# Optimization experiments

Hardware: AMD Instinct MI355X
Metric: run time of the kernel (lower is better)

## Reference

```python
import jax, jax.numpy as jnp
import numpy as np
import math

N_HEADS = 12


def setup_inputs() -> dict:
    key = jax.random.key(0)
    ks = jax.random.split(key, 6)
    B, S, DIM = 4, 2048, 768
    h = jax.random.normal(ks[0], (B, S, DIM), dtype=jnp.float32)
    attn_mask = jnp.ones((B, 1, 1, S), dtype=jnp.int32)
    scale = 1.0 / math.sqrt(DIM)
    wq = jax.random.normal(ks[1], (DIM, DIM), dtype=jnp.float32) * scale
    wk = jax.random.normal(ks[2], (DIM, DIM), dtype=jnp.float32) * scale
    wv = jax.random.normal(ks[3], (DIM, DIM), dtype=jnp.float32) * scale
    wo = jax.random.normal(ks[4], (DIM, DIM), dtype=jnp.float32) * scale
    return {"h": h, "attn_mask": attn_mask, "wq": wq, "wk": wk, "wv": wv, "wo": wo}


def reference(h, attn_mask, wq, wk, wv, wo):
    B, S, dim = h.shape
    H = N_HEADS
    D = dim // H
    qk_scale = 1.0 / math.sqrt(D)
    # NOTE: original uses .view(B, H, S, D) on the [B, S, H*D] projection —
    # a raw reshape, NOT the usual (B,S,H,D)->(B,H,S,D) transpose. Reproduce exactly.
    hq = (h @ wq.T).reshape(B, H, S, D)
    hk = (h @ wk.T).reshape(B, H, S, D)
    hv = (h @ wv.T).reshape(B, H, S, D)
    scores = jnp.einsum("bhqd,bhkd->bhqk", hq, hk) * qk_scale  # [B,H,S,S]
    scores = jnp.where(attn_mask == 0, -jnp.inf, scores)
    attn = jax.nn.softmax(scores.astype(jnp.float32), axis=-1)
    ctx = jnp.einsum("bhqk,bhkd->bhqd", attn, hv)  # [B,H,S,D]
    # dropout is identity in eval mode
    ctx = ctx.reshape(B, S, H * D)
    return ctx @ wo.T
```

## Files before the change

### kernel.cpp

```cpp
#include <hip/hip_runtime.h>
#include <math.h>

typedef __bf16 bf16x8 __attribute__((ext_vector_type(8)));
typedef float  f32x4  __attribute__((ext_vector_type(4)));
typedef float  f32x16 __attribute__((ext_vector_type(16)));

#define MFMA16(a, b, c) __builtin_amdgcn_mfma_f32_16x16x32_bf16((a), (b), (c), 0, 0, 0)
#define MFMA32(a, b, c) __builtin_amdgcn_mfma_f32_32x32x16_bf16((a), (b), (c), 0, 0, 0)

__device__ __forceinline__ unsigned short f2bf(float f) {
    unsigned int u = __float_as_uint(f);
    u += 0x7fffu + ((u >> 16) & 1u);
    return (unsigned short)(u >> 16);
}

__device__ __forceinline__ void gll16(const unsigned short* g, unsigned short* l) {
    __builtin_amdgcn_global_load_lds(
        (const __attribute__((address_space(1))) unsigned int*)g,
        (__attribute__((address_space(3))) unsigned int*)l, 16, 0, 0);
}

__global__ __launch_bounds__(256) void convert_kernel(
    const float* __restrict__ h, const float* __restrict__ wq,
    const float* __restrict__ wk, const float* __restrict__ wv,
    const float* __restrict__ wo,
    unsigned short* __restrict__ hb, unsigned short* __restrict__ wb)
{
    const int NH4 = 1572864;
    const int NW4 = 147456;
    int i4 = blockIdx.x * 256 + threadIdx.x;
    const float4* src;
    unsigned short* dst;
    int off;
    float sc = 1.0f;
    if (i4 < NH4) {
        src = (const float4*)h; dst = hb; off = i4;
    } else {
        int j = i4 - NH4;
        int w = j / NW4;
        off = j - w * NW4;
        const float* s = (w == 0) ? wq : (w == 1) ? wk : (w == 2) ? wv : wo;
        if (w == 0) sc = 0.18033688011112042f;
        src = (const float4*)s;
        dst = wb + w * 589824;
    }
    float4 v = src[off];
    ushort4 o;
    o.x = f2bf(v.x * sc); o.y = f2bf(v.y * sc);
    o.z = f2bf(v.z * sc); o.w = f2bf(v.w * sc);
    ((ushort4*)dst)[off] = o;
}

template <typename OutT>
__global__ __launch_bounds__(256) void gemm_bt(
    const unsigned short* __restrict__ A,
    const unsigned short* __restrict__ Bm,
    OutT* __restrict__ C)
{
    constexpr int K = 768, N = 768;
    __shared__ unsigned short As[2][128 * 32];
    __shared__ unsigned short Bs[2][128 * 32];
    const unsigned short* Bz = Bm + (size_t)blockIdx.z * N * K;
    OutT* Cz = C + (size_t)blockIdx.z * 8192 * N;

    const int tid  = threadIdx.x;
    const int bm   = blockIdx.x * 128, bn = blockIdx.y * 128;
    const int wave = tid >> 6, lane = tid & 63;
    const int wm   = (wave & 1) * 64, wn = (wave >> 1) * 64;
    const int l16  = lane & 15, quad = lane >> 4;

    const int sr  = tid >> 2;
    const int sp8 = ((tid & 3) ^ (sr & 3)) * 8;
    const int slot8 = (quad ^ (l16 & 3)) * 8;

    auto stage = [&](int k0, int bi) {
        gll16(A  + (size_t)(bm + sr) * K      + k0 + sp8, As[bi] + tid * 8);
        gll16(A  + (size_t)(bm + 64 + sr) * K + k0 + sp8, As[bi] + 2048 + tid * 8);
        gll16(Bz + (size_t)(bn + sr) * K      + k0 + sp8, Bs[bi] + tid * 8);
        gll16(Bz + (size_t)(bn + 64 + sr) * K + k0 + sp8, Bs[bi] + 2048 + tid * 8);
    };

    f32x4 acc[4][4] = {};

    stage(0, 0);
    __syncthreads();

    for (int i = 0; i < 24; i++) {
        const int cur = i & 1;
        if (i < 23) stage((i + 1) * 32, cur ^ 1);

        bf16x8 af[4], bfv[4];
        #pragma unroll
        for (int ii = 0; ii < 4; ii++)
            af[ii] = *(const bf16x8*)(As[cur] + (wm + ii * 16 + l16) * 32 + slot8);
        #pragma unroll
        for (int jj = 0; jj < 4; jj++)
            bfv[jj] = *(const bf16x8*)(Bs[cur] + (wn + jj * 16 + l16) * 32 + slot8);
        #pragma unroll
        for (int ii = 0; ii < 4; ii++)
            #pragma unroll
            for (int jj = 0; jj < 4; jj++)
                acc[ii][jj] = MFMA16(af[ii], bfv[jj], acc[ii][jj]);

        __syncthreads();
    }

    #pragma unroll
    for (int ii = 0; ii < 4; ii++) {
        #pragma unroll
        for (int jj = 0; jj < 4; jj++) {
            int row0 = bm + wm + ii * 16 + quad * 4;
            int col  = bn + wn + jj * 16 + l16;
            #pragma unroll
            for (int r = 0; r < 4; r++) {
                float v = acc[ii][jj][r];
                size_t idx = (size_t)(row0 + r) * N + col;
                if constexpr (sizeof(OutT) == 2) Cz[idx] = f2bf(v);
                else                             Cz[idx] = v;
            }
        }
    }
}

__global__ __launch_bounds__(256) void vtrans_kernel(
    const unsigned short* __restrict__ Vg,
    unsigned short* __restrict__ vt)
{
    constexpr int LDT = 72;
    __shared__ unsigned short Ts[64 * LDT];
    const int b = blockIdx.z, hh = blockIdx.y, kp0 = blockIdx.x * 64;
    const int tid = threadIdx.x;
    const size_t boff = (size_t)b * (24576 * 64);
    const int rowV0 = hh * 2048 + kp0;

    #pragma unroll
    for (int rep = 0; rep < 2; rep++) {
        int idx = rep * 256 + tid;
        int r = idx >> 3, dp = (idx & 7) * 8;
        uint4 v = *(const uint4*)(Vg + boff + (size_t)(rowV0 + r) * 64 + dp);
        unsigned short tmp[8];
        *(uint4*)tmp = v;
        #pragma unroll
        for (int i = 0; i < 8; i++) Ts[(dp + i) * LDT + r] = tmp[i];
    }
    __syncthreads();
    unsigned short* vtb = vt + ((size_t)(b * 12 + hh)) * 64 * 2048;
    #pragma unroll
    for (int rep = 0; rep < 2; rep++) {
        int idx = rep * 256 + tid;
        int d = idx >> 3, kp = (idx & 7) * 8;
        uint4 v = *(const uint4*)(Ts + d * LDT + kp);
        *(uint4*)(vtb + (size_t)d * 2048 + kp0 + kp) = v;
    }
}

__global__ __launch_bounds__(256) void attn_kernel(
    const unsigned short* __restrict__ Qg,
    const unsigned short* __restrict__ Kg,
    const unsigned short* __restrict__ vt,
    const int* __restrict__ mask,
    unsigned short* __restrict__ Og)
{
    __shared__ unsigned short Qs[128 * 64];
    __shared__ unsigned short Ks[2][64 * 64];
    __shared__ unsigned short Vs[2][64 * 64];
    __shared__ unsigned long long msh[32];

    const int b = blockIdx.z, hh = blockIdx.y, qt = blockIdx.x;
    const int tid  = threadIdx.x;
    const int wave = tid >> 6, lane = tid & 63;
    const int c31  = lane & 31, h = lane >> 5;
    const size_t boff = (size_t)b * (24576 * 64);
    const int rowQ0 = hh * 2048 + qt * 128;
    const int rowK0 = hh * 2048;
    const unsigned short* vtg = vt + ((size_t)(b * 12 + hh)) * 64 * 2048;
    const int sw = c31 & 7;

    const int srow = tid >> 3;
    const int sch8 = ((tid & 7) ^ (srow & 7)) * 8;

    auto stageKV = [&](int kt, int bi) {
        #pragma unroll
        for (int i = 0; i < 2; i++) {
            int row = i * 32 + srow;
            gll16(Kg  + boff + (size_t)(rowK0 + kt * 64 + row) * 64 + sch8,
                  Ks[bi] + i * 2048 + tid * 8);
            gll16(vtg + (size_t)row * 2048 + kt * 64 + sch8,
                  Vs[bi] + i * 2048 + tid * 8);
        }
    };

    #pragma unroll
    for (int i = 0; i < 4; i++) {
        int row = i * 32 + srow;
        gll16(Qg + boff + (size_t)(rowQ0 + row) * 64 + sch8, Qs + i * 2048 + tid * 8);
    }
    stageKV(0, 0);

    {
        const int4 a = *(const int4*)(mask + b * 2048 + tid * 8);
        const int4 c = *(const int4*)(mask + b * 2048 + tid * 8 + 4);
        unsigned char byte =
            (a.x != 0 ? 1u : 0u)       | (a.y != 0 ? 2u : 0u) |
            (a.z != 0 ? 4u : 0u)       | (a.w != 0 ? 8u : 0u) |
            (c.x != 0 ? 16u : 0u)      | (c.y != 0 ? 32u : 0u) |
            (c.z != 0 ? 64u : 0u)      | (c.w != 0 ? 128u : 0u);
        ((unsigned char*)msh)[tid] = byte;
    }
    __syncthreads();

    bf16x8 qf[4];
    #pragma unroll
    for (int c = 0; c < 4; c++) {
        int ch = (2 * c + h) ^ sw;
        qf[c] = *(const bf16x8*)(Qs + (wave * 32 + c31) * 64 + ch * 8);
    }

    f32x16 acc[2] = {};
    float l_run = 0.f;

    for (int kt = 0; kt < 32; kt++) {
        const int cur = kt & 1;
        if (kt < 31) stageKV(kt + 1, cur ^ 1);

        const unsigned long long am = msh[kt];

        f32x16 sT[2];
        #pragma unroll
        for (int t2 = 0; t2 < 2; t2++) {
            f32x16 z = {};
            #pragma unroll
            for (int c = 0; c < 4; c++) {
                int ch = (2 * c + h) ^ sw;
                bf16x8 kf = *(const bf16x8*)(Ks[cur] + (t2 * 32 + c31) * 64 + ch * 8);
                z = MFMA32(kf, qf[c], z);
            }
            sT[t2] = z;
        }

        unsigned int p01[2][4], p23[2][4];
        if (am == ~0ull) {
            #pragma unroll
            for (int t2 = 0; t2 < 2; t2++) {
                #pragma unroll
                for (int s = 0; s < 4; s++) {
                    float e0 = __builtin_amdgcn_exp2f(sT[t2][4*s+0]);
                    float e1 = __builtin_amdgcn_exp2f(sT[t2][4*s+1]);
                    float e2 = __builtin_amdgcn_exp2f(sT[t2][4*s+2]);
                    float e3 = __builtin_amdgcn_exp2f(sT[t2][4*s+3]);
                    unsigned int u0 = __float_as_uint(e0) & 0xffff0000u;
                    unsigned int u1 = __float_as_uint(e1) & 0xffff0000u;
                    unsigned int u2 = __float_as_uint(e2) & 0xffff0000u;
                    unsigned int u3 = __float_as_uint(e3) & 0xffff0000u;
                    l_run += __uint_as_float(u0) + __uint_as_float(u1)
                           + __uint_as_float(u2) + __uint_as_float(u3);
                    p01[t2][s] = __builtin_amdgcn_perm(u1, u0, 0x07060302u);
                    p23[t2][s] = __builtin_amdgcn_perm(u3, u2, 0x07060302u);
                }
            }
        } else {
            #pragma unroll
            for (int t2 = 0; t2 < 2; t2++) {
                #pragma unroll
                for (int s = 0; s < 4; s++) {
                    unsigned int nib = (unsigned int)(am >> (t2 * 32 + 8 * s + 4 * h)) & 0xFu;
                    float e0 = __builtin_amdgcn_exp2f(sT[t2][4*s+0]);
                    float e1 = __builtin_amdgcn_exp2f(sT[t2][4*s+1]);
                    float e2 = __builtin_amdgcn_exp2f(sT[t2][4*s+2]);
                    float e3 = __builtin_amdgcn_exp2f(sT[t2][4*s+3]);
                    e0 = (nib & 1u) ? e0 : 0.f;
                    e1 = (nib & 2u) ? e1 : 0.f;
                    e2 = (nib & 4u) ? e2 : 0.f;
                    e3 = (nib & 8u) ? e3 : 0.f;
                    unsigned int u0 = __float_as_uint(e0) & 0xffff0000u;
                    unsigned int u1 = __float_as_uint(e1) & 0xffff0000u;
                    unsigned int u2 = __float_as_uint(e2) & 0xffff0000u;
                    unsigned int u3 = __float_as_uint(e3) & 0xffff0000u;
                    l_run += __uint_as_float(u0) + __uint_as_float(u1)
                           + __uint_as_float(u2) + __uint_as_float(u3);
                    p01[t2][s] = __builtin_amdgcn_perm(u1, u0, 0x07060302u);
                    p23[t2][s] = __builtin_amdgcn_perm(u3, u2, 0x07060302u);
                }
            }
        }

        #pragma unroll
        for (int q = 0; q < 4; q++) {
            int t = q >> 1, p = q & 1;
            unsigned int L01 = h ? p01[t][2*p+1] : p01[t][2*p];
            unsigned int L23 = h ? p23[t][2*p+1] : p23[t][2*p];
            unsigned int pre01 = h ? p01[t][2*p] : p01[t][2*p+1];
            unsigned int pre23 = h ? p23[t][2*p] : p23[t][2*p+1];
            unsigned int P01 = (unsigned int)__shfl((int)pre01, lane ^ 32, 64);
            unsigned int P23 = (unsigned int)__shfl((int)pre23, lane ^ 32, 64);
            uint4 pfu;
            pfu.x = h ? P01 : L01;
            pfu.y = h ? P23 : L23;
            pfu.z = h ? L01 : P01;
            pfu.w = h ? L23 : P23;
            bf16x8 pf;
            __builtin_memcpy(&pf, &pfu, 16);
            #pragma unroll
            for (int nt = 0; nt < 2; nt++) {
                int ch = (2 * q + h) ^ sw;
                bf16x8 vf = *(const bf16x8*)(Vs[cur] + (nt * 32 + c31) * 64 + ch * 8);
                acc[nt] = MFMA32(pf, vf, acc[nt]);
            }
        }

        __syncthreads();
    }

    float lt = l_run + __shfl_xor(l_run, 32, 64);
    float linv = 1.0f / lt;
    #pragma unroll
    for (int reg = 0; reg < 16; reg++) {
        int rowfn = (reg & 3) + 8 * (reg >> 2) + 4 * h;
        float li = __shfl(linv, rowfn, 64);
        int row = rowQ0 + wave * 32 + rowfn;
        #pragma unroll
        for (int nt = 0; nt < 2; nt++)
            Og[boff + (size_t)row * 64 + nt * 32 + c31] = f2bf(acc[nt][reg] * li);
    }
}

extern "C" void kernel_launch(void* const* d_in, const int* in_sizes, int n_in,
                              void* d_out, int out_size, void* d_ws, size_t ws_size,
                              hipStream_t stream)
{
    const float* h    = (const float*)d_in[0];
    const int*   mask = (const int*)d_in[1];
    const float* wq   = (const float*)d_in[2];
    const float* wk   = (const float*)d_in[3];
    const float* wv   = (const float*)d_in[4];
    const float* wo   = (const float*)d_in[5];

    unsigned short* hb  = (unsigned short*)d_ws;
    unsigned short* wb  = hb + 6291456;
    unsigned short* qkv = wb + 4 * 589824;
    unsigned short* ctx = qkv + (size_t)3 * 6291456;

    convert_kernel<<<8448, 256, 0, stream>>>(h, wq, wk, wv, wo, hb, wb);
    gemm_bt<unsigned short><<<dim3(64, 6, 3), 256, 0, stream>>>(hb, wb, qkv);
    vtrans_kernel<<<dim3(32, 12, 4), 256, 0, stream>>>(qkv + (size_t)2 * 6291456, hb);
    attn_kernel<<<dim3(16, 12, 4), 256, 0, stream>>>(
        qkv, qkv + 6291456, hb, mask, ctx);
    gemm_bt<float><<<dim3(64, 6, 1), 256, 0, stream>>>(
        ctx, wb + (size_t)3 * 589824, (float*)d_out);
}
```

Measured before the change: 257.1 us.

## Use packed bf16 convert, permlane32 swap, and MFMA row-sum for softmax denominator

Replaces the manual truncate-and-perm bf16 packing of exponentials with v_cvt_pk_bf16_f32, which also switches rounding from truncation to round-to-nearest. Replaces the cross-half __shfl exchange with v_permlane32_swap_b32. Computes the softmax denominator by running an extra MFMA of P against a ones vector instead of scalar per-lane accumulation and shuffles. This removes VALU adds, bpermute traffic and the final shuffle, at the cost of one extra MFMA per step and a 16-register accumulator.

```diff
diff --git a/kernel.cpp b/kernel.cpp
--- a/kernel.cpp
+++ b/kernel.cpp
@@ -217,7 +217,10 @@
     }
 
     f32x16 acc[2] = {};
-    float l_run = 0.f;
+    f32x16 acc_l  = {};
+    bf16x8 onesf;
+    #pragma unroll
+    for (int i = 0; i < 8; i++) onesf[i] = (__bf16)1.0f;
 
     for (int kt = 0; kt < 32; kt++) {
         const int cur = kt & 1;
@@ -248,14 +251,10 @@
                     float e1 = __builtin_amdgcn_exp2f(sT[t2][4*s+1]);
                     float e2 = __builtin_amdgcn_exp2f(sT[t2][4*s+2]);
                     float e3 = __builtin_amdgcn_exp2f(sT[t2][4*s+3]);
-                    unsigned int u0 = __float_as_uint(e0) & 0xffff0000u;
-                    unsigned int u1 = __float_as_uint(e1) & 0xffff0000u;
-                    unsigned int u2 = __float_as_uint(e2) & 0xffff0000u;
-                    unsigned int u3 = __float_as_uint(e3) & 0xffff0000u;
-                    l_run += __uint_as_float(u0) + __uint_as_float(u1)
-                           + __uint_as_float(u2) + __uint_as_float(u3);
-                    p01[t2][s] = __builtin_amdgcn_perm(u1, u0, 0x07060302u);
-                    p23[t2][s] = __builtin_amdgcn_perm(u3, u2, 0x07060302u);
+                    asm("v_cvt_pk_bf16_f32 %0, %1, %2"
+                        : "=v"(p01[t2][s]) : "v"(e0), "v"(e1));
+                    asm("v_cvt_pk_bf16_f32 %0, %1, %2"
+                        : "=v"(p23[t2][s]) : "v"(e2), "v"(e3));
                 }
             }
         } else {
@@ -272,14 +271,10 @@
                     e1 = (nib & 2u) ? e1 : 0.f;
                     e2 = (nib & 4u) ? e2 : 0.f;
                     e3 = (nib & 8u) ? e3 : 0.f;
-                    unsigned int u0 = __float_as_uint(e0) & 0xffff0000u;
-                    unsigned int u1 = __float_as_uint(e1) & 0xffff0000u;
-                    unsigned int u2 = __float_as_uint(e2) & 0xffff0000u;
-                    unsigned int u3 = __float_as_uint(e3) & 0xffff0000u;
-                    l_run += __uint_as_float(u0) + __uint_as_float(u1)
-                           + __uint_as_float(u2) + __uint_as_float(u3);
-                    p01[t2][s] = __builtin_amdgcn_perm(u1, u0, 0x07060302u);
-                    p23[t2][s] = __builtin_amdgcn_perm(u3, u2, 0x07060302u);
+                    asm("v_cvt_pk_bf16_f32 %0, %1, %2"
+                        : "=v"(p01[t2][s]) : "v"(e0), "v"(e1));
+                    asm("v_cvt_pk_bf16_f32 %0, %1, %2"
+                        : "=v"(p23[t2][s]) : "v"(e2), "v"(e3));
                 }
             }
         }
@@ -287,17 +282,15 @@
         #pragma unroll
         for (int q = 0; q < 4; q++) {
             int t = q >> 1, p = q & 1;
-            unsigned int L01 = h ? p01[t][2*p+1] : p01[t][2*p];
-            unsigned int L23 = h ? p23[t][2*p+1] : p23[t][2*p];
-            unsigned int pre01 = h ? p01[t][2*p] : p01[t][2*p+1];
-            unsigned int pre23 = h ? p23[t][2*p] : p23[t][2*p+1];
-            unsigned int P01 = (unsigned int)__shfl((int)pre01, lane ^ 32, 64);
-            unsigned int P23 = (unsigned int)__shfl((int)pre23, lane ^ 32, 64);
+            unsigned int a01 = p01[t][2 * p], b01 = p01[t][2 * p + 1];
+            unsigned int a23 = p23[t][2 * p], b23 = p23[t][2 * p + 1];
+            asm("v_permlane32_swap_b32 %0, %1" : "+v"(a01), "+v"(b01));
+            asm("v_permlane32_swap_b32 %0, %1" : "+v"(a23), "+v"(b23));
             uint4 pfu;
-            pfu.x = h ? P01 : L01;
-            pfu.y = h ? P23 : L23;
-            pfu.z = h ? L01 : P01;
-            pfu.w = h ? L23 : P23;
+            pfu.x = a01;
+            pfu.y = a23;
+            pfu.z = b01;
+            pfu.w = b23;
             bf16x8 pf;
             __builtin_memcpy(&pf, &pfu, 16);
             #pragma unroll
@@ -306,17 +299,16 @@
                 bf16x8 vf = *(const bf16x8*)(Vs[cur] + (nt * 32 + c31) * 64 + ch * 8);
                 acc[nt] = MFMA32(pf, vf, acc[nt]);
             }
+            acc_l = MFMA32(pf, onesf, acc_l);
         }
 
         __syncthreads();
     }
 
-    float lt = l_run + __shfl_xor(l_run, 32, 64);
-    float linv = 1.0f / lt;
     #pragma unroll
     for (int reg = 0; reg < 16; reg++) {
         int rowfn = (reg & 3) + 8 * (reg >> 2) + 4 * h;
-        float li = __shfl(linv, rowfn, 64);
+        float li = __builtin_amdgcn_rcpf(acc_l[reg]);
         int row = rowQ0 + wave * 32 + rowfn;
         #pragma unroll
         for (int nt = 0; nt < 2; nt++)
```

Result: no change. 258.2 us (+0.4%).
